# Kernel optimization log

Hardware: AMD Instinct MI355X
Metric: run time of the kernel (lower is better)

## Reference

```python
import jax, jax.numpy as jnp
import numpy as np

B, O, I, F, KS, H, W = 32, 64, 64, 16, 3, 128, 128


def setup_inputs() -> dict:
    key = jax.random.key(0)
    k1, k2, k3, k4 = jax.random.split(key, 4)
    addresses = jax.random.normal(k1, (B, O, I + 1, F), dtype=jnp.float32)
    x = jax.random.normal(k2, (B, I, H, W), dtype=jnp.float32)
    # kaiming-uniform-ish init for the (F, ks, ks) filter bank
    fan_in = KS * KS
    bound_w = np.sqrt(6.0 / ((1 + 5.0) * fan_in))  # kaiming_uniform a=sqrt(5)
    w_bank = jax.random.uniform(k3, (F, KS, KS), minval=-bound_w, maxval=bound_w, dtype=jnp.float32)
    bound_b = 1.0 / np.sqrt(fan_in)
    b_bank = jax.random.uniform(k4, (F,), minval=-bound_b, maxval=bound_b, dtype=jnp.float32)
    return {"addresses": addresses, "x": x, "w_bank": w_bank, "b_bank": b_bank, "s": 1, "p": 1}


def reference(addresses, x, w_bank, b_bank, s, p):
    # addresses: (B, O, I+1, F); slice off the bias address on dim 2
    w_addr = addresses[:, :, 1:]   # (B, O, I, F)
    b_addr = addresses[:, :, 0]    # (B, O, F)
    # soft routing over the filter bank (softmax over num_filters)
    aw = jax.nn.softmax(w_addr, axis=-1)
    w = jnp.einsum('boif,fkl->boikl', aw, w_bank)  # per-sample conv weights (B, O, I, ks, ks)
    ab = jax.nn.softmax(b_addr, axis=-1)
    b = jnp.einsum('bof,f->bo', ab, b_bank)        # per-sample bias (B, O)

    def conv_one(xi, wi):
        # xi: (I, H, W), wi: (O, I, ks, ks)
        y = jax.lax.conv_general_dilated(
            xi[None], wi, window_strides=(s, s),
            padding=[(p, p), (p, p)],
            dimension_numbers=('NCHW', 'OIHW', 'NCHW'))
        return y[0]  # (O, H', W')

    y = jax.vmap(conv_one)(x, w)  # per-example dynamic conv (groups=batch)
    return y + b[:, :, None, None]
```

## Files before the change

kernel.cpp:

```cpp
#include <hip/hip_runtime.h>

#define BB 32
#define OO 64
#define II 64
#define FF 16
#define HH 128
#define WW 128

typedef __attribute__((ext_vector_type(8))) __bf16 bf16x8;
typedef __attribute__((ext_vector_type(4))) float f32x4;

typedef __attribute__((address_space(3))) uint8_t  lds_u8;
typedef __attribute__((address_space(1))) const uint8_t g_u8;

__global__ __launch_bounds__(64)
void gen_weights(const float* __restrict__ addr,
                 const float* __restrict__ w_bank,
                 const float* __restrict__ b_bank,
                 __bf16* __restrict__ wT,
                 float* __restrict__ bias_out) {
    const int bo  = blockIdx.x;
    const int tid = threadIdx.x;

    __shared__ float bank_s[FF * 9];
    __shared__ float bbank_s[FF];
    for (int idx = tid; idx < FF * 9; idx += 64) bank_s[idx] = w_bank[idx];
    if (tid < FF) bbank_s[tid] = b_bank[tid];
    __syncthreads();

    const float* arow = addr + ((size_t)bo * (II + 1) + 1 + tid) * FF;
    float a[FF];
    float m = -1e30f;
#pragma unroll
    for (int f = 0; f < FF; ++f) { a[f] = arow[f]; m = fmaxf(m, a[f]); }
    float s = 0.f;
#pragma unroll
    for (int f = 0; f < FF; ++f) { a[f] = __expf(a[f] - m); s += a[f]; }
    const float inv = 1.0f / s;

    const int b = bo >> 6, o = bo & 63;
#pragma unroll
    for (int kl = 0; kl < 9; ++kl) {
        float acc = 0.f;
#pragma unroll
        for (int f = 0; f < FF; ++f) acc += a[f] * bank_s[f * 9 + kl];
        wT[(((size_t)b * 9 + kl) * OO + o) * II + tid] = (__bf16)(acc * inv);
    }

    if (tid == 0) {
        const float* brow = addr + (size_t)bo * (II + 1) * FF;
        float bb[FF];
        float bm = -1e30f;
#pragma unroll
        for (int f = 0; f < FF; ++f) { bb[f] = brow[f]; bm = fmaxf(bm, bb[f]); }
        float bs = 0.f;
#pragma unroll
        for (int f = 0; f < FF; ++f) { bb[f] = __expf(bb[f] - bm); bs += bb[f]; }
        float acc = 0.f;
#pragma unroll
        for (int f = 0; f < FF; ++f) acc += bb[f] * bbank_s[f];
        bias_out[bo] = acc / bs;
    }
}

#define SLOTB 8448
#define RINGOFF 73728
#define LDSZ (RINGOFF + 8 * SLOTB)

#define LOADPAIR(q_) do {                                                          \
    const int pxg_ = ph * 64 + l - 1;                                              \
    const bool okpx_ = (unsigned)pxg_ < 128u;                                      \
    _Pragma("unroll")                                                              \
    for (int j_ = 0; j_ < 2; ++j_) {                                               \
        const int rr_ = R0 + 2 * (q_) + j_ - 1;                                    \
        const bool ok_ = okpx_ && ((unsigned)rr_ < 128u);                          \
        const float* xs_ = xb + ((size_t)(wv * 8) * HH + rr_) * WW + pxg_;         \
        float* dst_ = j_ ? sm1 : sm0;                                              \
        _Pragma("unroll")                                                          \
        for (int jj_ = 0; jj_ < 8; ++jj_) {                                        \
            float v_ = 0.f;                                                        \
            if (ok_) v_ = xs_[(size_t)jj_ * (HH * WW)];                            \
            dst_[jj_] = v_;                                                        \
        }                                                                          \
    }                                                                              \
    {        \
        const int lr_ = l >> 4;                                                    \
        const int cc_ = (l >> 1) & 7;                                              \
        const int pxl_ = 64 + (l & 1);                                             \
        const int pxg2_ = ph * 64 + pxl_ - 1;                                      \
        const int rr_ = R0 + 2 * (q_) + lr_ - 1;                                   \
        const bool ok_ = (t < 32) && ((unsigned)pxg2_ < 128u)                      \
                         && ((unsigned)rr_ < 128u);                                \
        const float* xs_ = xb + ((size_t)(cc_ * 8) * HH + rr_) * WW + pxg2_;       \
        _Pragma("unroll")                                                          \
        for (int jj_ = 0; jj_ < 8; ++jj_) {                                        \
            float v_ = 0.f;                                                        \
            if (ok_) v_ = xs_[(size_t)jj_ * (HH * WW)];                            \
            smt[jj_] = v_;                                                         \
        }                                                                          \
    }                                                                              \
} while (0)

#define WRITEPAIR(q_) do {                                                         \
    bf16x8 u_;                                                                     \
    _Pragma("unroll")                                                              \
    for (int jj_ = 0; jj_ < 8; ++jj_) u_[jj_] = (__bf16)sm0[jj_];                  \
    *(bf16x8*)(LDS + RINGOFF + ((2 * (q_)) & 7) * SLOTB + l * 128                  \
               + ((wv ^ (l & 7)) << 4)) = u_;                                      \
    _Pragma("unroll")                                                              \
    for (int jj_ = 0; jj_ < 8; ++jj_) u_[jj_] = (__bf16)sm1[jj_];                  \
    *(bf16x8*)(LDS + RINGOFF + ((2 * (q_) + 1) & 7) * SLOTB + l * 128              \
               + ((wv ^ (l & 7)) << 4)) = u_;                                      \
    if (t < 32) {                                                                  \
        const int lr_ = l >> 4;                                                    \
        const int cc_ = (l >> 1) & 7;                                              \
        const int pxl_ = 64 + (l & 1);                                             \
        _Pragma("unroll")                                                          \
        for (int jj_ = 0; jj_ < 8; ++jj_) u_[jj_] = (__bf16)smt[jj_];              \
        *(bf16x8*)(LDS + RINGOFF + ((2 * (q_) + lr_) & 7) * SLOTB + pxl_ * 128     \
                   + ((cc_ ^ (pxl_ & 7)) << 4)) = u_;                              \
    }                                                                              \
} while (0)

__global__ __launch_bounds__(512, 2)
void conv_fused(const float* __restrict__ x, const __bf16* __restrict__ wT,
                const float* __restrict__ bias, float* __restrict__ y) {
    __shared__ __align__(16) char LDS[LDSZ];

    const int hwid = blockIdx.x;
    const int work = (hwid & 7) * 32 + (hwid >> 3);
    const int b  = work >> 3;
    const int r3 = work & 7;
    const int ph = r3 >> 2;
    const int rg = r3 & 3;
    const int R0 = rg * 32;

    const int t  = threadIdx.x;
    const int wv = t >> 6;
    const int l  = t & 63;
    const int lm = l & 15;
    const int lk = l >> 4;
    const int oh = wv >> 2;
    const int g  = wv & 3;

    const __bf16* wb = wT + (size_t)b * 9 * OO * II;
    const float*  xb = x + (size_t)b * II * HH * WW;

#pragma unroll
    for (int it = 0; it < 9; ++it) {
        const int cid = it * 512 + t;
        const int kl  = cid >> 9;
        const int rem = cid & 511;
        const int o   = rem >> 3;
        const int c   = rem & 7;
        const __bf16* src = wb + ((kl * 64 + o) << 6) + ((c ^ (o & 7)) << 3);
        __builtin_amdgcn_global_load_lds((g_u8*)src,
            (lds_u8*)(LDS + (size_t)(it * 512 + (t & 448)) * 16), 16, 0, 0);
    }

    float sm0[8], sm1[8], smt[8];

    LOADPAIR(0);
    WRITEPAIR(0);
    LOADPAIR(1);
    WRITEPAIR(1);

    float bbias[2][4];
    {
        const float* bp = bias + b * OO;
#pragma unroll
        for (int mf = 0; mf < 2; ++mf)
#pragma unroll
            for (int r = 0; r < 4; ++r)
                bbias[mf][r] = bp[oh * 32 + mf * 16 + lk * 4 + r];
    }
    f32x4 acc[2][2];
#pragma unroll
    for (int mf = 0; mf < 2; ++mf)
#pragma unroll
        for (int nf = 0; nf < 2; ++nf)
#pragma unroll
            for (int r = 0; r < 4; ++r)
                acc[mf][nf][r] = bbias[mf][r];

    __syncthreads();

    const int pxbase = g * 16 + lm;
    const int obase0 = oh * 32 + lm;
    int s0 = 0;

    for (int p = 0; p < 16; ++p) {
        if (p < 15) LOADPAIR(p + 2);

#pragma unroll
        for (int ks = 0; ks < 18; ++ks) {
            const int kl = ks >> 1, k0 = ks & 1;
            const int dr = kl / 3, dc = kl - 3 * dr;
            const int cc = lk + 4 * k0;
            bf16x8 af[2], bv[2];
#pragma unroll
            for (int mf = 0; mf < 2; ++mf) {
                const int aaddr = kl * 8192 + (obase0 + mf * 16) * 128
                                + ((cc ^ (lm & 7)) << 4);
                af[mf] = *(const bf16x8*)(LDS + aaddr);
            }
            const int lpx = pxbase + dc;
#pragma unroll
            for (int nf = 0; nf < 2; ++nf) {
                const int slot = (s0 + nf + dr) & 7;
                const int baddr = RINGOFF + slot * SLOTB + lpx * 128
                                + ((cc ^ (lpx & 7)) << 4);
                bv[nf] = *(const bf16x8*)(LDS + baddr);
            }
#pragma unroll
            for (int mf = 0; mf < 2; ++mf)
#pragma unroll
                for (int nf = 0; nf < 2; ++nf)
                    acc[mf][nf] = __builtin_amdgcn_mfma_f32_16x16x32_bf16(
                        af[mf], bv[nf], acc[mf][nf], 0, 0, 0);
        }

        if (p < 15) WRITEPAIR(p + 2);

        __syncthreads();

#pragma unroll
        for (int mf = 0; mf < 2; ++mf)
#pragma unroll
            for (int r = 0; r < 4; ++r) {
                const int o = oh * 32 + mf * 16 + lk * 4 + r;
#pragma unroll
                for (int nf = 0; nf < 2; ++nf) {
                    const int rowg = R0 + 2 * p + nf;
                    y[(((size_t)b * OO + o) * HH + rowg) * WW + ph * 64 + pxbase]
                        = acc[mf][nf][r];
                }
            }
#pragma unroll
        for (int mf = 0; mf < 2; ++mf)
#pragma unroll
            for (int nf = 0; nf < 2; ++nf)
#pragma unroll
                for (int r = 0; r < 4; ++r)
                    acc[mf][nf][r] = bbias[mf][r];

        s0 = (s0 + 2) & 7;
    }
}

extern "C" void kernel_launch(void* const* d_in, const int* in_sizes, int n_in,
                              void* d_out, int out_size, void* d_ws, size_t ws_size,
                              hipStream_t stream) {
    const float* addresses = (const float*)d_in[0];
    const float* x         = (const float*)d_in[1];
    const float* w_bank    = (const float*)d_in[2];
    const float* b_bank    = (const float*)d_in[3];
    float* out = (float*)d_out;

    float*  bias_ws = (float*)d_ws;
    __bf16* wT      = (__bf16*)((char*)d_ws + 8192);

    gen_weights<<<BB * OO, 64, 0, stream>>>(addresses, w_bank, b_bank, wT, bias_ws);
    conv_fused<<<256, 512, 0, stream>>>(x, wT, bias_ws, out);
}
```

Measured before the change: 77.30 us.

## Compute four output rows per iteration with a ten-slot input ring buffer

Each loop iteration now produces four output rows instead of two, using a 2x4 MFMA accumulator tile. Each weight fragment loaded from LDS is therefore reused across more rows, and the number of block-wide barriers is halved. The row ring buffer grows from 8 to 10 slots with modulo slot offsets. Two row-pair prefetches are split across the two halves of the k loop to overlap global loads with MFMAs. This raises register and LDS use, which could reduce occupancy below two blocks per CU.

```diff
diff --git a/kernel.cpp b/kernel.cpp
--- a/kernel.cpp
+++ b/kernel.cpp
@@ -64,17 +64,18 @@
 }
 
 #define SLOTB 8448
+#define NSLOT 10
 #define RINGOFF 73728
-#define LDSZ (RINGOFF + 8 * SLOTB)
-
-#define LOADPAIR(q_) do {                                                          \
+#define LDSZ (RINGOFF + NSLOT * SLOTB)
+
+#define LOADPAIR(pr_) do {                                                         \
     const int pxg_ = ph * 64 + l - 1;                                              \
     const bool okpx_ = (unsigned)pxg_ < 128u;                                      \
     _Pragma("unroll")                                                              \
     for (int j_ = 0; j_ < 2; ++j_) {                                               \
-        const int rr_ = R0 + 2 * (q_) + j_ - 1;                                    \
-        const bool ok_ = okpx_ && ((unsigned)rr_ < 128u);                          \
-        const float* xs_ = xb + ((size_t)(wv * 8) * HH + rr_) * WW + pxg_;         \
+        const int gr_ = R0 + (pr_) + j_ - 1;                                       \
+        const bool ok_ = okpx_ && ((unsigned)gr_ < 128u);                          \
+        const float* xs_ = xb + ((size_t)(wv * 8) * HH + gr_) * WW + pxg_;         \
         float* dst_ = j_ ? sm1 : sm0;                                              \
         _Pragma("unroll")                                                          \
         for (int jj_ = 0; jj_ < 8; ++jj_) {                                        \
@@ -83,15 +84,15 @@
             dst_[jj_] = v_;                                                        \
         }                                                                          \
     }                                                                              \
-    {        \
+    {               \
         const int lr_ = l >> 4;                                                    \
         const int cc_ = (l >> 1) & 7;                                              \
         const int pxl_ = 64 + (l & 1);                                             \
         const int pxg2_ = ph * 64 + pxl_ - 1;                                      \
-        const int rr_ = R0 + 2 * (q_) + lr_ - 1;                                   \
+        const int gr_ = R0 + (pr_) + lr_ - 1;                                      \
         const bool ok_ = (t < 32) && ((unsigned)pxg2_ < 128u)                      \
-                         && ((unsigned)rr_ < 128u);                                \
-        const float* xs_ = xb + ((size_t)(cc_ * 8) * HH + rr_) * WW + pxg2_;       \
+                         && ((unsigned)gr_ < 128u);                                \
+        const float* xs_ = xb + ((size_t)(cc_ * 8) * HH + gr_) * WW + pxg2_;       \
         _Pragma("unroll")                                                          \
         for (int jj_ = 0; jj_ < 8; ++jj_) {                                        \
             float v_ = 0.f;                                                        \
@@ -101,24 +102,50 @@
     }                                                                              \
 } while (0)
 
-#define WRITEPAIR(q_) do {                                                         \
+#define WRITEPAIR(sA_, sB_) do {                                                   \
     bf16x8 u_;                                                                     \
     _Pragma("unroll")                                                              \
     for (int jj_ = 0; jj_ < 8; ++jj_) u_[jj_] = (__bf16)sm0[jj_];                  \
-    *(bf16x8*)(LDS + RINGOFF + ((2 * (q_)) & 7) * SLOTB + l * 128                  \
+    *(bf16x8*)(LDS + RINGOFF + (sA_) * SLOTB + l * 128                             \
                + ((wv ^ (l & 7)) << 4)) = u_;                                      \
     _Pragma("unroll")                                                              \
     for (int jj_ = 0; jj_ < 8; ++jj_) u_[jj_] = (__bf16)sm1[jj_];                  \
-    *(bf16x8*)(LDS + RINGOFF + ((2 * (q_) + 1) & 7) * SLOTB + l * 128              \
+    *(bf16x8*)(LDS + RINGOFF + (sB_) * SLOTB + l * 128                             \
                + ((wv ^ (l & 7)) << 4)) = u_;                                      \
     if (t < 32) {                                                                  \
         const int lr_ = l >> 4;                                                    \
         const int cc_ = (l >> 1) & 7;                                              \
         const int pxl_ = 64 + (l & 1);                                             \
+        const int sl_ = lr_ ? (sB_) : (sA_);                                       \
         _Pragma("unroll")                                                          \
         for (int jj_ = 0; jj_ < 8; ++jj_) u_[jj_] = (__bf16)smt[jj_];              \
-        *(bf16x8*)(LDS + RINGOFF + ((2 * (q_) + lr_) & 7) * SLOTB + pxl_ * 128     \
+        *(bf16x8*)(LDS + RINGOFF + sl_ * SLOTB + pxl_ * 128                        \
                    + ((cc_ ^ (pxl_ & 7)) << 4)) = u_;                              \
+    }                                                                              \
+} while (0)
+
+#define KS_RANGE(K0_, K1_) do {                                                    \
+    _Pragma("unroll")                                                              \
+    for (int ks = (K0_); ks < (K1_); ++ks) {                                       \
+        const int kl = ks >> 1, k0 = ks & 1;                                       \
+        const int dr = kl / 3, dc = kl - 3 * dr;                                   \
+        const int cc = lk + 4 * k0;                                                \
+        bf16x8 af[2], bv[4];                                                       \
+        _Pragma("unroll")                                                          \
+        for (int mf = 0; mf < 2; ++mf)                                             \
+            af[mf] = *(const bf16x8*)(LDS + kl * 8192 + (obase0 + mf * 16) * 128   \
+                                      + ((cc ^ (lm & 7)) << 4));                   \
+        const int lpx = pxbase + dc;                                               \
+        const int swb = lpx * 128 + ((cc ^ (lpx & 7)) << 4);                       \
+        _Pragma("unroll")                                                          \
+        for (int nf = 0; nf < 4; ++nf)                                             \
+            bv[nf] = *(const bf16x8*)(LDS + off_[nf + dr] + swb);                  \
+        _Pragma("unroll")                                                          \
+        for (int mf = 0; mf < 2; ++mf)                                             \
+            _Pragma("unroll")                                                      \
+            for (int nf = 0; nf < 4; ++nf)                                         \
+                acc[mf][nf] = __builtin_amdgcn_mfma_f32_16x16x32_bf16(             \
+                    af[mf], bv[nf], acc[mf][nf], 0, 0, 0);                         \
     }                                                                              \
 } while (0)
 
@@ -160,10 +187,9 @@
 
     float sm0[8], sm1[8], smt[8];
 
-    LOADPAIR(0);
-    WRITEPAIR(0);
-    LOADPAIR(1);
-    WRITEPAIR(1);
+    LOADPAIR(0); WRITEPAIR(0, 1);
+    LOADPAIR(2); WRITEPAIR(2, 3);
+    LOADPAIR(4); WRITEPAIR(4, 5);
 
     float bbias[2][4];
     {
@@ -174,11 +200,11 @@
             for (int r = 0; r < 4; ++r)
                 bbias[mf][r] = bp[oh * 32 + mf * 16 + lk * 4 + r];
     }
-    f32x4 acc[2][2];
+    f32x4 acc[2][4];
 #pragma unroll
     for (int mf = 0; mf < 2; ++mf)
 #pragma unroll
-        for (int nf = 0; nf < 2; ++nf)
+        for (int nf = 0; nf < 4; ++nf)
 #pragma unroll
             for (int r = 0; r < 4; ++r)
                 acc[mf][nf][r] = bbias[mf][r];
@@ -187,40 +213,27 @@
 
     const int pxbase = g * 16 + lm;
     const int obase0 = oh * 32 + lm;
+
     int s0 = 0;
-
-    for (int p = 0; p < 16; ++p) {
-        if (p < 15) LOADPAIR(p + 2);
-
-#pragma unroll
-        for (int ks = 0; ks < 18; ++ks) {
-            const int kl = ks >> 1, k0 = ks & 1;
-            const int dr = kl / 3, dc = kl - 3 * dr;
-            const int cc = lk + 4 * k0;
-            bf16x8 af[2], bv[2];
-#pragma unroll
-            for (int mf = 0; mf < 2; ++mf) {
-                const int aaddr = kl * 8192 + (obase0 + mf * 16) * 128
-                                + ((cc ^ (lm & 7)) << 4);
-                af[mf] = *(const bf16x8*)(LDS + aaddr);
-            }
-            const int lpx = pxbase + dc;
-#pragma unroll
-            for (int nf = 0; nf < 2; ++nf) {
-                const int slot = (s0 + nf + dr) & 7;
-                const int baddr = RINGOFF + slot * SLOTB + lpx * 128
-                                + ((cc ^ (lpx & 7)) << 4);
-                bv[nf] = *(const bf16x8*)(LDS + baddr);
-            }
-#pragma unroll
-            for (int mf = 0; mf < 2; ++mf)
-#pragma unroll
-                for (int nf = 0; nf < 2; ++nf)
-                    acc[mf][nf] = __builtin_amdgcn_mfma_f32_16x16x32_bf16(
-                        af[mf], bv[nf], acc[mf][nf], 0, 0, 0);
+    for (int p = 0; p < 8; ++p) {
+        int off_[6];
+#pragma unroll
+        for (int d = 0; d < 6; ++d) {
+            int ss = s0 + d; if (ss >= NSLOT) ss -= NSLOT;
+            off_[d] = RINGOFF + ss * SLOTB;
         }
-
-        if (p < 15) WRITEPAIR(p + 2);
+        int wA = s0 + 6; if (wA >= NSLOT) wA -= NSLOT;
+        int wB = wA + 1; if (wB >= NSLOT) wB -= NSLOT;
+        int wC = wB + 1; if (wC >= NSLOT) wC -= NSLOT;
+        int wD = wC + 1; if (wD >= NSLOT) wD -= NSLOT;
+        const int pr = 4 * p;
+        const bool pf = (p < 7);
+
+        if (pf) LOADPAIR(pr + 6);
+        KS_RANGE(0, 9);
+        if (pf) { WRITEPAIR(wA, wB); LOADPAIR(pr + 8); }
+        KS_RANGE(9, 18);
+        if (pf) WRITEPAIR(wC, wD);
 
         __syncthreads();
 
@@ -230,8 +243,8 @@
             for (int r = 0; r < 4; ++r) {
                 const int o = oh * 32 + mf * 16 + lk * 4 + r;
 #pragma unroll
-                for (int nf = 0; nf < 2; ++nf) {
-                    const int rowg = R0 + 2 * p + nf;
+                for (int nf = 0; nf < 4; ++nf) {
+                    const int rowg = R0 + pr + nf;
                     y[(((size_t)b * OO + o) * HH + rowg) * WW + ph * 64 + pxbase]
                         = acc[mf][nf][r];
                 }
@@ -239,12 +252,12 @@
 #pragma unroll
         for (int mf = 0; mf < 2; ++mf)
 #pragma unroll
-            for (int nf = 0; nf < 2; ++nf)
+            for (int nf = 0; nf < 4; ++nf)
 #pragma unroll
                 for (int r = 0; r < 4; ++r)
                     acc[mf][nf][r] = bbias[mf][r];
 
-        s0 = (s0 + 2) & 7;
+        s0 += 4; if (s0 >= NSLOT) s0 -= NSLOT;
     }
 }
 
```

Measured after the change: 96.31 us. +24.6%, slower.

## Use 1024-thread blocks computing four output rows per step with a 10-slot ring

Applied to the files above, without the earlier changes.

The conv kernel moves from 512 to 1024 threads per block at one block per CU. Each step now produces four output rows instead of two, with warps split by row and half-row, and the input ring buffer grows from 8 to 10 slots. The aim is to halve the number of loop iterations and barriers and to reuse the weight tile in LDS across more rows. The cost is larger barriers across 16 waves, less scope for overlap between blocks, and more LDS per block.

```diff
diff --git a/kernel.cpp b/kernel.cpp
--- a/kernel.cpp
+++ b/kernel.cpp
@@ -64,17 +64,20 @@
 }
 
 #define SLOTB 8448
-#define RINGOFF 73728
-#define LDSZ (RINGOFF + 8 * SLOTB)
-
-#define LOADPAIR(q_) do {                                                          \
-    const int pxg_ = ph * 64 + l - 1;                                              \
+#define NSLOT 10
+#define RING  73728
+#define LDSZ (RING + NSLOT * SLOTB)
+
+#define LOADPAIRH(p0_, tl_) do {                                                   \
+    const int ll_  = (tl_) & 63;                                                   \
+    const int wvl_ = (tl_) >> 6;                                                   \
+    const int pxg_ = ph * 64 + ll_ - 1;                                            \
     const bool okpx_ = (unsigned)pxg_ < 128u;                                      \
     _Pragma("unroll")                                                              \
     for (int j_ = 0; j_ < 2; ++j_) {                                               \
-        const int rr_ = R0 + 2 * (q_) + j_ - 1;                                    \
-        const bool ok_ = okpx_ && ((unsigned)rr_ < 128u);                          \
-        const float* xs_ = xb + ((size_t)(wv * 8) * HH + rr_) * WW + pxg_;         \
+        const int grow_ = R0 + (p0_) + j_ - 1;                                     \
+        const bool ok_ = okpx_ && ((unsigned)grow_ < 128u);                        \
+        const float* xs_ = xb + ((size_t)(wvl_ * 8) * HH + grow_) * WW + pxg_;     \
         float* dst_ = j_ ? sm1 : sm0;                                              \
         _Pragma("unroll")                                                          \
         for (int jj_ = 0; jj_ < 8; ++jj_) {                                        \
@@ -83,15 +86,15 @@
             dst_[jj_] = v_;                                                        \
         }                                                                          \
     }                                                                              \
-    {        \
-        const int lr_ = l >> 4;                                                    \
-        const int cc_ = (l >> 1) & 7;                                              \
-        const int pxl_ = 64 + (l & 1);                                             \
+    {                           \
+        const int lr_ = ((tl_) >> 4) & 1;                                          \
+        const int cc_ = ((tl_) >> 1) & 7;                                          \
+        const int pxl_ = 64 + ((tl_) & 1);                                         \
         const int pxg2_ = ph * 64 + pxl_ - 1;                                      \
-        const int rr_ = R0 + 2 * (q_) + lr_ - 1;                                   \
-        const bool ok_ = (t < 32) && ((unsigned)pxg2_ < 128u)                      \
-                         && ((unsigned)rr_ < 128u);                                \
-        const float* xs_ = xb + ((size_t)(cc_ * 8) * HH + rr_) * WW + pxg2_;       \
+        const int grow_ = R0 + (p0_) + lr_ - 1;                                    \
+        const bool ok_ = ((tl_) < 32) && ((unsigned)pxg2_ < 128u)                  \
+                         && ((unsigned)grow_ < 128u);                              \
+        const float* xs_ = xb + ((size_t)(cc_ * 8) * HH + grow_) * WW + pxg2_;     \
         _Pragma("unroll")                                                          \
         for (int jj_ = 0; jj_ < 8; ++jj_) {                                        \
             float v_ = 0.f;                                                        \
@@ -101,28 +104,31 @@
     }                                                                              \
 } while (0)
 
-#define WRITEPAIR(q_) do {                                                         \
+#define WRITEPAIRH(sA_, sB_, tl_) do {                                             \
+    const int ll_  = (tl_) & 63;                                                   \
+    const int wvl_ = (tl_) >> 6;                                                   \
     bf16x8 u_;                                                                     \
     _Pragma("unroll")                                                              \
     for (int jj_ = 0; jj_ < 8; ++jj_) u_[jj_] = (__bf16)sm0[jj_];                  \
-    *(bf16x8*)(LDS + RINGOFF + ((2 * (q_)) & 7) * SLOTB + l * 128                  \
-               + ((wv ^ (l & 7)) << 4)) = u_;                                      \
+    *(bf16x8*)(LDS + RING + (sA_) * SLOTB + ll_ * 128                              \
+               + ((wvl_ ^ (ll_ & 7)) << 4)) = u_;                                  \
     _Pragma("unroll")                                                              \
     for (int jj_ = 0; jj_ < 8; ++jj_) u_[jj_] = (__bf16)sm1[jj_];                  \
-    *(bf16x8*)(LDS + RINGOFF + ((2 * (q_) + 1) & 7) * SLOTB + l * 128              \
-               + ((wv ^ (l & 7)) << 4)) = u_;                                      \
-    if (t < 32) {                                                                  \
-        const int lr_ = l >> 4;                                                    \
-        const int cc_ = (l >> 1) & 7;                                              \
-        const int pxl_ = 64 + (l & 1);                                             \
+    *(bf16x8*)(LDS + RING + (sB_) * SLOTB + ll_ * 128                              \
+               + ((wvl_ ^ (ll_ & 7)) << 4)) = u_;                                  \
+    if ((tl_) < 32) {                                                              \
+        const int lr_ = ((tl_) >> 4) & 1;                                          \
+        const int cc_ = ((tl_) >> 1) & 7;                                          \
+        const int pxl_ = 64 + ((tl_) & 1);                                         \
+        const int sl_ = lr_ ? (sB_) : (sA_);                                       \
         _Pragma("unroll")                                                          \
         for (int jj_ = 0; jj_ < 8; ++jj_) u_[jj_] = (__bf16)smt[jj_];              \
-        *(bf16x8*)(LDS + RINGOFF + ((2 * (q_) + lr_) & 7) * SLOTB + pxl_ * 128     \
+        *(bf16x8*)(LDS + RING + sl_ * SLOTB + pxl_ * 128                           \
                    + ((cc_ ^ (pxl_ & 7)) << 4)) = u_;                              \
     }                                                                              \
 } while (0)
 
-__global__ __launch_bounds__(512, 2)
+__global__ __launch_bounds__(1024, 1)
 void conv_fused(const float* __restrict__ x, const __bf16* __restrict__ wT,
                 const float* __restrict__ bias, float* __restrict__ y) {
     __shared__ __align__(16) char LDS[LDSZ];
@@ -136,34 +142,46 @@
     const int R0 = rg * 32;
 
     const int t  = threadIdx.x;
-    const int wv = t >> 6;
+    const int w  = t >> 6;
     const int l  = t & 63;
     const int lm = l & 15;
     const int lk = l >> 4;
-    const int oh = wv >> 2;
-    const int g  = wv & 3;
+    const int oh = w >> 3;
+    const int w7 = w & 7;
+    const int r  = w7 >> 1;
+    const int q  = w7 & 1;
 
     const __bf16* wb = wT + (size_t)b * 9 * OO * II;
     const float*  xb = x + (size_t)b * II * HH * WW;
 
-#pragma unroll
-    for (int it = 0; it < 9; ++it) {
-        const int cid = it * 512 + t;
-        const int kl  = cid >> 9;
-        const int rem = cid & 511;
-        const int o   = rem >> 3;
-        const int c   = rem & 7;
-        const __bf16* src = wb + ((kl * 64 + o) << 6) + ((c ^ (o & 7)) << 3);
-        __builtin_amdgcn_global_load_lds((g_u8*)src,
-            (lds_u8*)(LDS + (size_t)(it * 512 + (t & 448)) * 16), 16, 0, 0);
+    const int obase0 = oh * 32 + lm;
+
+#pragma unroll
+    for (int it = 0; it < 5; ++it) {
+        const int gbase = it * 1024 + (t & 960);
+        if (gbase < 4608) {
+            const int cid = it * 1024 + t;
+            const int kl  = cid >> 9;
+            const int rem = cid & 511;
+            const int o   = rem >> 3;
+            const int c   = rem & 7;
+            const __bf16* src = wb + ((kl * 64 + o) << 6) + ((c ^ (o & 7)) << 3);
+            __builtin_amdgcn_global_load_lds((g_u8*)src,
+                (lds_u8*)(LDS + (size_t)gbase * 16), 16, 0, 0);
+        }
     }
 
     float sm0[8], sm1[8], smt[8];
 
-    LOADPAIR(0);
-    WRITEPAIR(0);
-    LOADPAIR(1);
-    WRITEPAIR(1);
+    if (t < 512) {
+        LOADPAIRH(0, t);
+        WRITEPAIRH(0, 1, t);
+        LOADPAIRH(4, t);
+        WRITEPAIRH(4, 5, t);
+    } else {
+        LOADPAIRH(2, t - 512);
+        WRITEPAIRH(2, 3, t - 512);
+    }
 
     float bbias[2][4];
     {
@@ -171,8 +189,8 @@
 #pragma unroll
         for (int mf = 0; mf < 2; ++mf)
 #pragma unroll
-            for (int r = 0; r < 4; ++r)
-                bbias[mf][r] = bp[oh * 32 + mf * 16 + lk * 4 + r];
+            for (int rr = 0; rr < 4; ++rr)
+                bbias[mf][rr] = bp[oh * 32 + mf * 16 + lk * 4 + rr];
     }
     f32x4 acc[2][2];
 #pragma unroll
@@ -180,17 +198,28 @@
 #pragma unroll
         for (int nf = 0; nf < 2; ++nf)
 #pragma unroll
-            for (int r = 0; r < 4; ++r)
-                acc[mf][nf][r] = bbias[mf][r];
+            for (int rr = 0; rr < 4; ++rr)
+                acc[mf][nf][rr] = bbias[mf][rr];
 
     __syncthreads();
 
-    const int pxbase = g * 16 + lm;
-    const int obase0 = oh * 32 + lm;
     int s0 = 0;
 
-    for (int p = 0; p < 16; ++p) {
-        if (p < 15) LOADPAIR(p + 2);
+    for (int p = 0; p < 8; ++p) {
+        int d0_ = s0 + r;  if (d0_ >= NSLOT) d0_ -= NSLOT;
+        int d1_ = d0_ + 1; if (d1_ >= NSLOT) d1_ -= NSLOT;
+        int d2_ = d1_ + 1; if (d2_ >= NSLOT) d2_ -= NSLOT;
+        const int o3[3] = { RING + d0_ * SLOTB, RING + d1_ * SLOTB,
+                            RING + d2_ * SLOTB };
+        int wA = s0 + 6; if (wA >= NSLOT) wA -= NSLOT;
+        int wB = wA + 1; if (wB >= NSLOT) wB -= NSLOT;
+        int wC = wB + 1; if (wC >= NSLOT) wC -= NSLOT;
+        int wD = wC + 1; if (wD >= NSLOT) wD -= NSLOT;
+
+        if (p < 7) {
+            if (t < 512) LOADPAIRH(4 * p + 6, t);
+            else         LOADPAIRH(4 * p + 8, t - 512);
+        }
 
 #pragma unroll
         for (int ks = 0; ks < 18; ++ks) {
@@ -199,18 +228,14 @@
             const int cc = lk + 4 * k0;
             bf16x8 af[2], bv[2];
 #pragma unroll
-            for (int mf = 0; mf < 2; ++mf) {
-                const int aaddr = kl * 8192 + (obase0 + mf * 16) * 128
-                                + ((cc ^ (lm & 7)) << 4);
-                af[mf] = *(const bf16x8*)(LDS + aaddr);
-            }
-            const int lpx = pxbase + dc;
+            for (int mf = 0; mf < 2; ++mf)
+                af[mf] = *(const bf16x8*)(LDS + kl * 8192
+                         + (obase0 + mf * 16) * 128 + ((cc ^ (lm & 7)) << 4));
 #pragma unroll
             for (int nf = 0; nf < 2; ++nf) {
-                const int slot = (s0 + nf + dr) & 7;
-                const int baddr = RINGOFF + slot * SLOTB + lpx * 128
-                                + ((cc ^ (lpx & 7)) << 4);
-                bv[nf] = *(const bf16x8*)(LDS + baddr);
+                const int lpx = q * 32 + nf * 16 + lm + dc;
+                bv[nf] = *(const bf16x8*)(LDS + o3[dr] + lpx * 128
+                         + ((cc ^ (lpx & 7)) << 4));
             }
 #pragma unroll
             for (int mf = 0; mf < 2; ++mf)
@@ -220,20 +245,24 @@
                         af[mf], bv[nf], acc[mf][nf], 0, 0, 0);
         }
 
-        if (p < 15) WRITEPAIR(p + 2);
+        if (p < 7) {
+            if (t < 512) WRITEPAIRH(wA, wB, t);
+            else         WRITEPAIRH(wC, wD, t - 512);
+        }
 
         __syncthreads();
 
+        const int row = R0 + 4 * p + r;
 #pragma unroll
         for (int mf = 0; mf < 2; ++mf)
 #pragma unroll
-            for (int r = 0; r < 4; ++r) {
-                const int o = oh * 32 + mf * 16 + lk * 4 + r;
+            for (int rr = 0; rr < 4; ++rr) {
+                const int o = oh * 32 + mf * 16 + lk * 4 + rr;
 #pragma unroll
                 for (int nf = 0; nf < 2; ++nf) {
-                    const int rowg = R0 + 2 * p + nf;
-                    y[(((size_t)b * OO + o) * HH + rowg) * WW + ph * 64 + pxbase]
-                        = acc[mf][nf][r];
+                    const int col = ph * 64 + q * 32 + nf * 16 + lm;
+                    y[(((size_t)b * OO + o) * HH + row) * WW + col]
+                        = acc[mf][nf][rr];
                 }
             }
 #pragma unroll
@@ -241,10 +270,10 @@
 #pragma unroll
             for (int nf = 0; nf < 2; ++nf)
 #pragma unroll
-                for (int r = 0; r < 4; ++r)
-                    acc[mf][nf][r] = bbias[mf][r];
-
-        s0 = (s0 + 2) & 7;
+                for (int rr = 0; rr < 4; ++rr)
+                    acc[mf][nf][rr] = bbias[mf][rr];
+
+        s0 += 4; if (s0 >= NSLOT) s0 -= NSLOT;
     }
 }
 
@@ -261,5 +290,5 @@
     __bf16* wT      = (__bf16*)((char*)d_ws + 8192);
 
     gen_weights<<<BB * OO, 64, 0, stream>>>(addresses, w_bank, b_bank, wT, bias_ws);
-    conv_fused<<<256, 512, 0, stream>>>(x, wT, bias_ws, out);
+    conv_fused<<<256, 1024, 0, stream>>>(x, wT, bias_ws, out);
 }
```

Measured after the change: 87.63 us. 13.4% more time.
